# Performance work log

Measured on AMD Instinct MI355X. Metric: run time of the kernel, lower is better.

The kernel has to match this reference:

```python
import jax, jax.numpy as jnp
import numpy as np

B, S, IN_F, OUT_F, GROUP = 2, 1024, 4096, 4096, 128
N_GROUPS = IN_F // GROUP  # 32


def setup_inputs() -> dict:
    key = jax.random.key(0)
    k1, k2, k3, k4 = jax.random.split(key, 4)
    x = jax.random.normal(k1, (B, S, IN_F), dtype=jnp.float32)
    # int4-range weights stored in int8, symmetric quant in [-7, 7]
    w_q = jax.random.randint(k2, (OUT_F, N_GROUPS, GROUP), -7, 8, dtype=jnp.int8)
    # per-(group, out_feature) scales, positive
    s_w = jax.random.uniform(k3, (N_GROUPS, OUT_F), dtype=jnp.float32,
                             minval=1e-3, maxval=2e-2)
    bias = jax.random.normal(k4, (OUT_F,), dtype=jnp.float32)
    return {"x": x, "w_q": w_q, "s_w": s_w, "bias": bias}


def reference(x, w_q, s_w, bias):
    # Faithful to QuantLinearW4Grouped.forward:
    #   y_g = einsum('ngk,ogk->ngo', x_f, w_f); y = (y_g * s_w[None]).sum(1) + bias
    # Expressed as a single fused einsum (identical math, no (n,g,o) intermediate).
    prefix = x.shape[:-1]
    orig_dtype = x.dtype
    xg = x.reshape(-1, N_GROUPS, GROUP).astype(jnp.float32)  # (n, g, k)
    w_f = w_q.astype(jnp.float32)                            # (o, g, k)
    y = jnp.einsum('ngk,ogk,go->no', xg, w_f, s_w)           # (n, o)
    y = y + bias.astype(y.dtype)
    return y.reshape(*prefix, OUT_F).astype(orig_dtype)
```

## Files before the change

kernel.cpp:

```cpp
#include <hip/hip_runtime.h>
#include <hip/hip_bf16.h>
#include <stdint.h>

#define M_TOK 2048
#define N_OUT 4096
#define K_IN  4096
#define GROUPSZ 128
#define NGRP  32

typedef signed char i8;
typedef int    intx4  __attribute__((ext_vector_type(4)));
typedef float  floatx4 __attribute__((ext_vector_type(4)));

#define AS1 __attribute__((address_space(1)))
#define AS3 __attribute__((address_space(3)))

#define XQ_BLOCKS (M_TOK)
#define WQ_BLOCKS (N_OUT * K_IN / 16 / 256)

__global__ __launch_bounds__(256) void quant_kernel(
    const float* __restrict__ x, const int* __restrict__ wq,
    i8* __restrict__ xq, i8* __restrict__ wq8, float* __restrict__ sx) {
  __shared__ float red[4];
  int b = blockIdx.x;
  int tid = threadIdx.x;
  if (b < XQ_BLOCKS) {
    const float* xr = x + (size_t)b * K_IN;
    int e0 = tid * 16;
    float4 v0 = *(const float4*)(xr + e0);
    float4 v1 = *(const float4*)(xr + e0 + 4);
    float4 v2 = *(const float4*)(xr + e0 + 8);
    float4 v3 = *(const float4*)(xr + e0 + 12);
    float m = fabsf(v0.x);
    m = fmaxf(m, fabsf(v0.y)); m = fmaxf(m, fabsf(v0.z)); m = fmaxf(m, fabsf(v0.w));
    m = fmaxf(m, fabsf(v1.x)); m = fmaxf(m, fabsf(v1.y)); m = fmaxf(m, fabsf(v1.z)); m = fmaxf(m, fabsf(v1.w));
    m = fmaxf(m, fabsf(v2.x)); m = fmaxf(m, fabsf(v2.y)); m = fmaxf(m, fabsf(v2.z)); m = fmaxf(m, fabsf(v2.w));
    m = fmaxf(m, fabsf(v3.x)); m = fmaxf(m, fabsf(v3.y)); m = fmaxf(m, fabsf(v3.z)); m = fmaxf(m, fabsf(v3.w));
#pragma unroll
    for (int off = 32; off > 0; off >>= 1)
      m = fmaxf(m, __shfl_xor(m, off, 64));
    int lane = tid & 63, wv = tid >> 6;
    if (lane == 0) red[wv] = m;
    __syncthreads();
    m = fmaxf(fmaxf(red[0], red[1]), fmaxf(red[2], red[3]));
    float inv = (m > 0.f) ? 127.f / m : 0.f;
    union { i8 q[16]; int4 v; } u;
    u.q[0]  = (i8)(int)rintf(v0.x * inv); u.q[1]  = (i8)(int)rintf(v0.y * inv);
    u.q[2]  = (i8)(int)rintf(v0.z * inv); u.q[3]  = (i8)(int)rintf(v0.w * inv);
    u.q[4]  = (i8)(int)rintf(v1.x * inv); u.q[5]  = (i8)(int)rintf(v1.y * inv);
    u.q[6]  = (i8)(int)rintf(v1.z * inv); u.q[7]  = (i8)(int)rintf(v1.w * inv);
    u.q[8]  = (i8)(int)rintf(v2.x * inv); u.q[9]  = (i8)(int)rintf(v2.y * inv);
    u.q[10] = (i8)(int)rintf(v2.z * inv); u.q[11] = (i8)(int)rintf(v2.w * inv);
    u.q[12] = (i8)(int)rintf(v3.x * inv); u.q[13] = (i8)(int)rintf(v3.y * inv);
    u.q[14] = (i8)(int)rintf(v3.z * inv); u.q[15] = (i8)(int)rintf(v3.w * inv);
    *(int4*)(xq + (size_t)b * K_IN + e0) = u.v;
    if (tid == 0) sx[b] = m * (1.f / 127.f);
  } else {
    size_t t = (size_t)(b - XQ_BLOCKS) * 256 + tid;
    size_t base = t * 16;
    const int* src = wq + base;
    int4 a0 = *(const int4*)(src);
    int4 a1 = *(const int4*)(src + 4);
    int4 a2 = *(const int4*)(src + 8);
    int4 a3 = *(const int4*)(src + 12);
    union { i8 q[16]; int4 v; } u;
    u.q[0]  = (i8)a0.x; u.q[1]  = (i8)a0.y; u.q[2]  = (i8)a0.z; u.q[3]  = (i8)a0.w;
    u.q[4]  = (i8)a1.x; u.q[5]  = (i8)a1.y; u.q[6]  = (i8)a1.z; u.q[7]  = (i8)a1.w;
    u.q[8]  = (i8)a2.x; u.q[9]  = (i8)a2.y; u.q[10] = (i8)a2.z; u.q[11] = (i8)a2.w;
    u.q[12] = (i8)a3.x; u.q[13] = (i8)a3.y; u.q[14] = (i8)a3.z; u.q[15] = (i8)a3.w;
    *(int4*)(wq8 + base) = u.v;
  }
}

#define BM 256
#define BN 128
#define BK 64
#define NT (K_IN / BK)

__global__ __launch_bounds__(512, 2) void gemm_i8_kernel(
    const i8* __restrict__ Aq, const i8* __restrict__ Bq,
    const float* __restrict__ sx, const float* __restrict__ sw,
    const float* __restrict__ bias, float* __restrict__ C) {
  __shared__ i8 As[2 * BM * BK];
  __shared__ i8 Bs[2 * BN * BK];
  __shared__ float sws[NGRP * BN];

  const int tid  = threadIdx.x;
  const int lane = tid & 63;
  const int wave = tid >> 6;
  const int quad = lane >> 4;
  const int l16  = lane & 15;
  const int bm = blockIdx.y;
  const int bn = blockIdx.x;
  const int wm = wave >> 1;
  const int wn = wave & 1;

  const int rowA0 = bm * BM;
  const int rowB0 = bn * BN;

  const int cA0 = tid, cA1 = 512 + tid, cB = tid;
  const i8* srcA0 = Aq + (size_t)(rowA0 + (cA0 >> 2)) * K_IN
                       + (((cA0 & 3) ^ ((cA0 >> 2) & 3)) << 4);
  const i8* srcA1 = Aq + (size_t)(rowA0 + (cA1 >> 2)) * K_IN
                       + (((cA1 & 3) ^ ((cA1 >> 2) & 3)) << 4);
  const i8* srcB0 = Bq + (size_t)(rowB0 + (cB >> 2)) * K_IN
                       + (((cB & 3) ^ ((cB >> 2) & 3)) << 4);
  i8* dstA0 = As + (size_t)(wave * 64) * 16;
  i8* dstA1 = As + (size_t)(512 + wave * 64) * 16;
  i8* dstB0 = Bs + (size_t)(wave * 64) * 16;

  auto stage = [&](int buf, int t) {
    const size_t ko = (size_t)t * BK;
    __builtin_amdgcn_global_load_lds(
        (const AS1 void*)(srcA0 + ko),
        (AS3 void*)(dstA0 + (size_t)buf * (BM * BK)), 16, 0, 0);
    __builtin_amdgcn_global_load_lds(
        (const AS1 void*)(srcA1 + ko),
        (AS3 void*)(dstA1 + (size_t)buf * (BM * BK)), 16, 0, 0);
    __builtin_amdgcn_global_load_lds(
        (const AS1 void*)(srcB0 + ko),
        (AS3 void*)(dstB0 + (size_t)buf * (BN * BK)), 16, 0, 0);
  };

  stage(0, 0);
  {
    int g = tid >> 4, c0 = (tid & 15) * 8;
    const float* src = sw + (size_t)g * N_OUT + rowB0 + c0;
    float* dst = sws + g * BN + c0;
    *(float4*)(dst)     = *(const float4*)(src);
    *(float4*)(dst + 4) = *(const float4*)(src + 4);
  }
  __syncthreads();

  floatx4 master[4][4];
#pragma unroll
  for (int i = 0; i < 4; ++i)
#pragma unroll
    for (int j = 0; j < 4; ++j) master[i][j] = (floatx4)0.0f;

  const intx4 MAGICV = {0x4B400000, 0x4B400000, 0x4B400000, 0x4B400000};
  const float MAGICF = 12582912.0f;

  const int xk = (quad ^ (l16 & 3)) << 4;

  for (int t = 0; t < NT; ++t) {
    const int cur = t & 1;
    if (t + 1 < NT) {
      stage(cur ^ 1, t + 1);
      asm volatile("s_waitcnt vmcnt(3)" ::: "memory");
    } else {
      asm volatile("s_waitcnt vmcnt(0)" ::: "memory");
    }
    __builtin_amdgcn_s_barrier();

    const i8* Ab = As + (size_t)cur * (BM * BK);
    const i8* Bb = Bs + (size_t)cur * (BN * BK);
    intx4 a[4], b[4];
#pragma unroll
    for (int i = 0; i < 4; ++i)
      a[i] = *(const intx4*)(Ab + (size_t)(wm * 64 + i * 16 + l16) * BK + xk);
#pragma unroll
    for (int j = 0; j < 4; ++j)
      b[j] = *(const intx4*)(Bb + (size_t)(wn * 64 + j * 16 + l16) * BK + xk);

    const int g = t >> 1;
    float swv[4];
#pragma unroll
    for (int j = 0; j < 4; ++j)
      swv[j] = sws[g * BN + wn * 64 + j * 16 + l16];

    asm volatile("s_waitcnt lgkmcnt(0)" ::: "memory");
    __builtin_amdgcn_s_barrier();

#pragma unroll
    for (int i = 0; i < 4; ++i)
#pragma unroll
      for (int j = 0; j < 4; ++j) {
        intx4 acc = __builtin_amdgcn_mfma_i32_16x16x64_i8(a[i], b[j], MAGICV, 0, 0, 0);
        master[i][j] += (__builtin_bit_cast(floatx4, acc) - MAGICF) * swv[j];
      }
  }

#pragma unroll
  for (int i = 0; i < 4; ++i) {
    float4 sxv = *(const float4*)(sx + rowA0 + wm * 64 + i * 16 + quad * 4);
#pragma unroll
    for (int j = 0; j < 4; ++j) {
      int col = rowB0 + wn * 64 + j * 16 + l16;
      float bv = bias[col];
      int rloc = wm * 64 + i * 16 + quad * 4;
      C[(size_t)(rowA0 + rloc + 0) * N_OUT + col] = master[i][j][0] * sxv.x + bv;
      C[(size_t)(rowA0 + rloc + 1) * N_OUT + col] = master[i][j][1] * sxv.y + bv;
      C[(size_t)(rowA0 + rloc + 2) * N_OUT + col] = master[i][j][2] * sxv.z + bv;
      C[(size_t)(rowA0 + rloc + 3) * N_OUT + col] = master[i][j][3] * sxv.w + bv;
    }
  }
}

extern "C" void kernel_launch(void* const* d_in, const int* in_sizes, int n_in,
                              void* d_out, int out_size, void* d_ws, size_t ws_size,
                              hipStream_t stream) {
  const float* x    = (const float*)d_in[0];
  const int*   wq   = (const int*)d_in[1];
  const float* sw   = (const float*)d_in[2];
  const float* bias = (const float*)d_in[3];
  float* out = (float*)d_out;

  i8*    xq  = (i8*)d_ws;
  i8*    wq8 = (i8*)((char*)d_ws + (size_t)M_TOK * K_IN);
  float* sx  = (float*)((char*)d_ws + (size_t)M_TOK * K_IN
                                     + (size_t)N_OUT * K_IN);

  {
    int nblocks = XQ_BLOCKS + WQ_BLOCKS;
    quant_kernel<<<nblocks, 256, 0, stream>>>(x, wq, xq, wq8, sx);
  }
  {
    dim3 grid(N_OUT / BN, M_TOK / BM);
    gemm_i8_kernel<<<grid, 512, 0, stream>>>(xq, wq8, sx, sw, bias, out);
  }
}
```

Measured before the change: 202.1 us.

## Widen K tile to a full quant group and chain two int8 MFMAs

Doubles BK from 64 to 128 so each K tile covers exactly one 128-wide scale group. Two int8 MFMAs are chained into one integer accumulator before the single magic-number float conversion and scaled FMA, which halves the dequant arithmetic and the barriers per group. The LDS swizzle and the global-to-LDS load mapping are reworked for 8 chunks per row, and the vmcnt wait is adjusted to match. Shared memory per block grows to roughly 112KB, which likely prevents the two blocks per CU that the launch bounds request.

```diff
diff --git a/kernel.cpp b/kernel.cpp
--- a/kernel.cpp
+++ b/kernel.cpp
@@ -74,7 +74,7 @@
 
 #define BM 256
 #define BN 128
-#define BK 64
+#define BK 128
 #define NT (K_IN / BK)
 
 __global__ __launch_bounds__(512, 2) void gemm_i8_kernel(
@@ -98,28 +98,39 @@
   const int rowA0 = bm * BM;
   const int rowB0 = bn * BN;
 
-  const int cA0 = tid, cA1 = 512 + tid, cB = tid;
-  const i8* srcA0 = Aq + (size_t)(rowA0 + (cA0 >> 2)) * K_IN
-                       + (((cA0 & 3) ^ ((cA0 >> 2) & 3)) << 4);
-  const i8* srcA1 = Aq + (size_t)(rowA0 + (cA1 >> 2)) * K_IN
-                       + (((cA1 & 3) ^ ((cA1 >> 2) & 3)) << 4);
-  const i8* srcB0 = Bq + (size_t)(rowB0 + (cB >> 2)) * K_IN
-                       + (((cB & 3) ^ ((cB >> 2) & 3)) << 4);
-  i8* dstA0 = As + (size_t)(wave * 64) * 16;
-  i8* dstA1 = As + (size_t)(512 + wave * 64) * 16;
-  i8* dstB0 = Bs + (size_t)(wave * 64) * 16;
+  const i8* srcA[4]; const i8* srcB[2];
+#pragma unroll
+  for (int i = 0; i < 4; ++i) {
+    int chunk = i * 512 + tid;
+    int row = chunk >> 3;
+    int csw = (chunk & 7) ^ (row & 7);
+    srcA[i] = Aq + (size_t)(rowA0 + row) * K_IN + (csw << 4);
+  }
+#pragma unroll
+  for (int i = 0; i < 2; ++i) {
+    int chunk = i * 512 + tid;
+    int row = chunk >> 3;
+    int csw = (chunk & 7) ^ (row & 7);
+    srcB[i] = Bq + (size_t)(rowB0 + row) * K_IN + (csw << 4);
+  }
+  i8* dstA[4]; i8* dstB[2];
+#pragma unroll
+  for (int i = 0; i < 4; ++i) dstA[i] = As + (size_t)(i * 512 + wave * 64) * 16;
+#pragma unroll
+  for (int i = 0; i < 2; ++i) dstB[i] = Bs + (size_t)(i * 512 + wave * 64) * 16;
 
   auto stage = [&](int buf, int t) {
     const size_t ko = (size_t)t * BK;
-    __builtin_amdgcn_global_load_lds(
-        (const AS1 void*)(srcA0 + ko),
-        (AS3 void*)(dstA0 + (size_t)buf * (BM * BK)), 16, 0, 0);
-    __builtin_amdgcn_global_load_lds(
-        (const AS1 void*)(srcA1 + ko),
-        (AS3 void*)(dstA1 + (size_t)buf * (BM * BK)), 16, 0, 0);
-    __builtin_amdgcn_global_load_lds(
-        (const AS1 void*)(srcB0 + ko),
-        (AS3 void*)(dstB0 + (size_t)buf * (BN * BK)), 16, 0, 0);
+#pragma unroll
+    for (int i = 0; i < 4; ++i)
+      __builtin_amdgcn_global_load_lds(
+          (const AS1 void*)(srcA[i] + ko),
+          (AS3 void*)(dstA[i] + (size_t)buf * (BM * BK)), 16, 0, 0);
+#pragma unroll
+    for (int i = 0; i < 2; ++i)
+      __builtin_amdgcn_global_load_lds(
+          (const AS1 void*)(srcB[i] + ko),
+          (AS3 void*)(dstB[i] + (size_t)buf * (BN * BK)), 16, 0, 0);
   };
 
   stage(0, 0);
@@ -141,13 +152,15 @@
   const intx4 MAGICV = {0x4B400000, 0x4B400000, 0x4B400000, 0x4B400000};
   const float MAGICF = 12582912.0f;
 
-  const int xk = (quad ^ (l16 & 3)) << 4;
+  const int h  = l16 & 7;
+  const int x0 = (quad ^ h) << 4;
+  const int x1 = x0 ^ 64;
 
   for (int t = 0; t < NT; ++t) {
     const int cur = t & 1;
     if (t + 1 < NT) {
       stage(cur ^ 1, t + 1);
-      asm volatile("s_waitcnt vmcnt(3)" ::: "memory");
+      asm volatile("s_waitcnt vmcnt(6)" ::: "memory");
     } else {
       asm volatile("s_waitcnt vmcnt(0)" ::: "memory");
     }
@@ -155,19 +168,24 @@
 
     const i8* Ab = As + (size_t)cur * (BM * BK);
     const i8* Bb = Bs + (size_t)cur * (BN * BK);
-    intx4 a[4], b[4];
-#pragma unroll
-    for (int i = 0; i < 4; ++i)
-      a[i] = *(const intx4*)(Ab + (size_t)(wm * 64 + i * 16 + l16) * BK + xk);
+    intx4 a[4][2], b[4][2];
+#pragma unroll
+    for (int i = 0; i < 4; ++i) {
+      const i8* pa = Ab + (size_t)(wm * 64 + i * 16 + l16) * BK;
+      a[i][0] = *(const intx4*)(pa + x0);
+      a[i][1] = *(const intx4*)(pa + x1);
+    }
+#pragma unroll
+    for (int j = 0; j < 4; ++j) {
+      const i8* pb = Bb + (size_t)(wn * 64 + j * 16 + l16) * BK;
+      b[j][0] = *(const intx4*)(pb + x0);
+      b[j][1] = *(const intx4*)(pb + x1);
+    }
+
+    float swv[4];
 #pragma unroll
     for (int j = 0; j < 4; ++j)
-      b[j] = *(const intx4*)(Bb + (size_t)(wn * 64 + j * 16 + l16) * BK + xk);
-
-    const int g = t >> 1;
-    float swv[4];
-#pragma unroll
-    for (int j = 0; j < 4; ++j)
-      swv[j] = sws[g * BN + wn * 64 + j * 16 + l16];
+      swv[j] = sws[t * BN + wn * 64 + j * 16 + l16];
 
     asm volatile("s_waitcnt lgkmcnt(0)" ::: "memory");
     __builtin_amdgcn_s_barrier();
@@ -176,7 +194,8 @@
     for (int i = 0; i < 4; ++i)
 #pragma unroll
       for (int j = 0; j < 4; ++j) {
-        intx4 acc = __builtin_amdgcn_mfma_i32_16x16x64_i8(a[i], b[j], MAGICV, 0, 0, 0);
+        intx4 acc = __builtin_amdgcn_mfma_i32_16x16x64_i8(a[i][0], b[j][0], MAGICV, 0, 0, 0);
+        acc = __builtin_amdgcn_mfma_i32_16x16x64_i8(a[i][1], b[j][1], acc, 0, 0, 0);
         master[i][j] += (__builtin_bit_cast(floatx4, acc) - MAGICF) * swv[j];
       }
   }
```

Measured after the change: 184.1 us. 8.9% less time.
